# Optimization experiments

Hardware: AMD Instinct MI355X
Metric: run time of the kernel (lower is better)

The kernel has to match this reference:

```python
import jax, jax.numpy as jnp
import numpy as np

HEIGHT, WIDTH = 32, 32
NUM_HEADS = 16
FREQUENCY = 10000.0


def _get_thetas(dim, height, width, frequency):
    # dim = head_dim, must be even. Returns (height*width, dim).
    half = dim // 2
    ifreq = 1.0 / (frequency ** (jnp.arange(half, dtype=jnp.float32) / half))
    freqs_h = jnp.arange(height, dtype=jnp.float32)[:, None] * ifreq[None, :]  # (h, half)
    freqs_w = jnp.arange(width, dtype=jnp.float32)[:, None] * ifreq[None, :]   # (w, half)
    theta_h = jnp.broadcast_to(freqs_h[:, None, :], (height, width, half))
    theta_w = jnp.broadcast_to(freqs_w[None, :, :], (height, width, half))
    theta = jnp.concatenate([theta_h, theta_w], axis=-1)  # (h, w, dim)
    return theta.reshape(height * width, dim)


def _add_rope(t, cos, sin):
    # t: (b, h, n, d); cos/sin: (n, d) broadcast over batch and heads
    x1, x2 = jnp.split(t, 2, axis=-1)
    t_rot = jnp.concatenate([-x2, x1], axis=-1)
    return t * cos + t_rot * sin


def setup_inputs() -> dict:
    key = jax.random.key(0)
    k1, k2, k3 = jax.random.split(key, 3)
    b, n, c = 8, HEIGHT * WIDTH, 1024
    tensor = jax.random.normal(k1, (b, n, c), dtype=jnp.float32)
    w_qkv = jax.random.normal(k2, (3 * c, c), dtype=jnp.float32) * (c ** -0.5)
    w_proj = jax.random.normal(k3, (c, c), dtype=jnp.float32) * (c ** -0.5)
    return {"tensor": tensor, "w_qkv": w_qkv, "w_proj": w_proj}


def reference(tensor, w_qkv, w_proj):
    b, n, c = tensor.shape
    hd = c // NUM_HEADS
    # QKV projection, split per-head last dim into q,k,v (matches torch chunk on dim=-1)
    qkv = jnp.einsum('bnc,fc->bnf', tensor, w_qkv)            # (b, n, 3c)
    qkv = qkv.reshape(b, n, NUM_HEADS, 3 * hd).transpose(0, 2, 1, 3)  # (b, H, n, 3*hd)
    q, k, v = jnp.split(qkv, 3, axis=-1)                      # each (b, H, n, hd)
    # 2D RoPE on q, k
    theta = _get_thetas(hd, HEIGHT, WIDTH, FREQUENCY).astype(tensor.dtype)  # (n, hd)
    cos, sin = jnp.cos(theta), jnp.sin(theta)
    q = _add_rope(q, cos, sin)
    k = _add_rope(k, cos, sin)
    # scaled dot product attention
    scale = hd ** -0.5
    scores = jnp.einsum('bhqd,bhkd->bhqk', q, k) * scale
    attn = jax.nn.softmax(scores, axis=-1)
    o = jnp.einsum('bhqk,bhkd->bhqd', attn, v)
    o = o.transpose(0, 2, 1, 3).reshape(b, n, c)
    return jnp.einsum('bnc,oc->bno', o, w_proj)
```

## Files before the change

### kernel.cpp

```cpp
#include <hip/hip_runtime.h>

typedef __attribute__((ext_vector_type(8))) short short8v;
typedef __attribute__((ext_vector_type(4))) float floatx4;
typedef __attribute__((ext_vector_type(4))) unsigned short ushortx4;

__device__ __forceinline__ unsigned int f2bf(float f){
  unsigned int u = __float_as_uint(f);
  u += 0x7fffu + ((u >> 16) & 1u);
  return u >> 16;
}

__device__ __forceinline__ void gload_lds16(const void* g, void* l){
  __builtin_amdgcn_global_load_lds((const __attribute__((address_space(1))) void*)g,
                                   (__attribute__((address_space(3))) void*)l, 16, 0, 0);
}

__global__ __launch_bounds__(256) void prep(
    const floatx4* __restrict__ t,  ushortx4* __restrict__ dt,
    const floatx4* __restrict__ wq, ushortx4* __restrict__ dq,
    const floatx4* __restrict__ wp, ushortx4* __restrict__ dp,
    float2* __restrict__ cs)
{
  int i = blockIdx.x * 256 + threadIdx.x;
  if(i < 3145728){
    const floatx4* s; ushortx4* d; int j;
    if(i < 2097152){ s = t;  d = dt; j = i; }
    else if(i < 2883584){ s = wq; d = dq; j = i - 2097152; }
    else { s = wp; d = dp; j = i - 2883584; }
    floatx4 v = s[j];
    ushortx4 o;
    #pragma unroll
    for(int k = 0; k < 4; ++k) o[k] = (unsigned short)f2bf(v[k]);
    d[j] = o;
  } else {
    int j = i - 3145728;
    int p = j >> 6, dd = j & 63;
    int y = p >> 5, x = p & 31;
    int dm = dd & 31;
    float ifr = powf(10000.0f, -(float)dm * (1.0f / 32.0f));
    float th = (float)(dd < 32 ? y : x) * ifr;
    cs[j].x = cosf(th);
    cs[j].y = sinf(th);
  }
}

template<int EPI>
__global__ __launch_bounds__(512, 2) void gemm8(
    const unsigned short* __restrict__ A,
    const unsigned short* __restrict__ B,
    int K, int N, int NXB,
    float* __restrict__ Cf,
    const float2* __restrict__ cs,
    unsigned short* __restrict__ qw,
    unsigned short* __restrict__ kw,
    unsigned short* __restrict__ vtw)
{
  __shared__ char lds[147456];
  const int tid = threadIdx.x;
  const int w = tid >> 6, lane = tid & 63;
  const int g = lane >> 4, c0 = lane & 15;
  const int wm = w >> 2, wn = w & 3;
  const int NT = K >> 6;

  const int per = gridDim.x >> 3;
  const int wg = (blockIdx.x & 7) * per + (blockIdx.x >> 3);
  const int by = wg / NXB, bx = wg % NXB;
  const size_t m0 = (size_t)by * 128;
  const size_t n0 = (size_t)bx * 256;

  const int row0 = tid >> 2;
  const int xch = (tid & 3) ^ ((tid >> 3) & 3);
  const unsigned short* sA0 = A + (m0 + row0) * K + xch * 8;
  const unsigned short* sB0 = B + (n0 + row0) * K + xch * 8;
  const unsigned short* sB1 = B + (n0 + row0 + 128) * K + xch * 8;
  const int wb = w * 1024;

  auto stT = [&](int t, char* bp){
    gload_lds16(sA0 + t * 64,      bp + wb);
    gload_lds16(sA0 + t * 64 + 32, bp + 8192 + wb);
    gload_lds16(sB0 + t * 64,      bp + 16384 + wb);
    gload_lds16(sB1 + t * 64,      bp + 24576 + wb);
    gload_lds16(sB0 + t * 64 + 32, bp + 32768 + wb);
    gload_lds16(sB1 + t * 64 + 32, bp + 40960 + wb);
  };

  const int archy = (g ^ ((c0 >> 1) & 3)) << 4;
  auto rdA = [&](const char* bp, int kh, int mf) -> short8v {
    return *(const short8v*)(bp + kh * 8192 + (wm * 64 + mf * 16 + c0) * 64 + archy);
  };
  auto rdB = [&](const char* bp, int kh, int nf) -> short8v {
    return *(const short8v*)(bp + 16384 + kh * 16384 + (wn * 64 + nf * 16 + c0) * 64 + archy);
  };

  floatx4 acc[4][4] = {};

  stT(0, lds);
  stT(1, lds + 49152);
  asm volatile("s_waitcnt vmcnt(6)" ::: "memory");
  __builtin_amdgcn_s_barrier();
  __builtin_amdgcn_sched_barrier(0);

  char* pa_ = lds;
  char* pb_ = lds + 49152;
  char* pc_ = lds + 98304;
  for(int t = 0; t < NT; ++t){
    const int tn2 = (t + 2 < NT) ? t + 2 : NT - 1;
    short8v amA[4], bnA[4], amB[4], bnB[4];
    #pragma unroll
    for(int nf = 0; nf < 4; ++nf) bnA[nf] = rdB(pa_, 0, nf);
    #pragma unroll
    for(int mf = 0; mf < 4; ++mf) amA[mf] = rdA(pa_, 0, mf);
    #pragma unroll
    for(int nf = 0; nf < 4; ++nf) bnB[nf] = rdB(pa_, 1, nf);
    #pragma unroll
    for(int mf = 0; mf < 4; ++mf) amB[mf] = rdA(pa_, 1, mf);
    stT(tn2, pc_);
    __builtin_amdgcn_sched_barrier(0);
    __builtin_amdgcn_s_setprio(1);
    #pragma unroll
    for(int mf = 0; mf < 4; ++mf)
      #pragma unroll
      for(int nf = 0; nf < 4; ++nf)
        acc[mf][nf] = __builtin_amdgcn_mfma_f32_16x16x32_bf16(amA[mf], bnA[nf], acc[mf][nf], 0, 0, 0);
    #pragma unroll
    for(int mf = 0; mf < 4; ++mf)
      #pragma unroll
      for(int nf = 0; nf < 4; ++nf)
        acc[mf][nf] = __builtin_amdgcn_mfma_f32_16x16x32_bf16(amB[mf], bnB[nf], acc[mf][nf], 0, 0, 0);
    __builtin_amdgcn_s_setprio(0);
    asm volatile("s_waitcnt vmcnt(6)" ::: "memory");
    __builtin_amdgcn_s_barrier();
    __builtin_amdgcn_sched_barrier(0);
    char* tmp = pa_; pa_ = pb_; pb_ = pc_; pc_ = tmp;
  }
  __syncthreads();

  if(EPI == 0){
    #pragma unroll
    for(int mf = 0; mf < 4; ++mf){
      size_t mrow = m0 + wm * 64 + mf * 16 + g * 4;
      #pragma unroll
      for(int nf = 0; nf < 4; ++nf){
        size_t n = n0 + wn * 64 + nf * 16 + c0;
        #pragma unroll
        for(int r = 0; r < 4; ++r)
          Cf[(mrow + r) * N + n] = acc[mf][nf][r];
      }
    }
  } else {
    int t = (int)(n0 >> 6) + wn;
    int sect = t % 3, hh = t / 3;
    if(sect == 2){
      #pragma unroll
      for(int mf = 0; mf < 4; ++mf){
        size_t m = m0 + wm * 64 + mf * 16 + g * 4;
        int b = (int)(m >> 10); int p = (int)(m & 1023);
        #pragma unroll
        for(int nf = 0; nf < 4; ++nf){
          int d = nf * 16 + c0;
          ushortx4 pk;
          #pragma unroll
          for(int r = 0; r < 4; ++r) pk[r] = (unsigned short)f2bf(acc[mf][nf][r]);
          *(ushortx4*)(vtw + ((size_t)(b * 16 + hh) * 64 + d) * 1024 + p) = pk;
        }
      }
    } else {
      unsigned short* dst = (sect == 0) ? qw : kw;
      const float qs = (sect == 0) ? 0.18033688011112042f : 1.0f;
      const int codd = c0 & 1;
      #pragma unroll
      for(int mf = 0; mf < 4; ++mf){
        #pragma unroll
        for(int r = 0; r < 4; ++r){
          size_t m = m0 + wm * 64 + mf * 16 + g * 4 + r;
          int b = (int)(m >> 10); int p = (int)(m & 1023);
          const float2* csr = cs + (size_t)p * 64;
          unsigned short* orow = dst + ((size_t)(b * 16 + hh) * 1024 + p) * 64;
          #pragma unroll
          for(int nf = 0; nf < 2; ++nf){
            int d = nf * 16 + c0;
            float x1 = acc[mf][nf][r], x2 = acc[mf][nf + 2][r];
            float2 cc1 = csr[d], cc2 = csr[d + 32];
            unsigned int u1 = f2bf((x1 * cc1.x - x2 * cc1.y) * qs);
            unsigned int u2 = f2bf((x2 * cc2.x + x1 * cc2.y) * qs);
            unsigned int p1 = (unsigned int)__shfl_xor((int)u1, 1);
            unsigned int p2 = (unsigned int)__shfl_xor((int)u2, 1);
            unsigned int val = codd ? (p2 | (u2 << 16)) : (u1 | (p1 << 16));
            int off = codd ? (d + 31) : d;
            *(unsigned int*)(orow + off) = val;
          }
        }
      }
    }
  }
}

__global__ __launch_bounds__(512, 4) void attn_kernel(
    const unsigned short* __restrict__ qw,
    const unsigned short* __restrict__ kw,
    const unsigned short* __restrict__ vtw,
    unsigned short* __restrict__ ow)
{
  __shared__ char smem[65536];
  const int tid = threadIdx.x;
  const int w = tid >> 6, lane = tid & 63;
  const int g = lane >> 4, c0 = lane & 15;
  const int bb = blockIdx.x;
  const int xcd = bb & 7, slot = bb >> 3;
  const int bh = xcd + ((slot >> 2) << 3);
  const int qt = slot & 3;
  const size_t bhoff = (size_t)bh * 1024 * 64;
  const unsigned short* Qb = qw + bhoff;
  const unsigned short* Kb = kw + bhoff;
  const unsigned short* Vb = vtw + bhoff;
  const int q0 = qt * 256 + w * 32;
  char* Pw = smem + 32768 + w * 4096;

  const int srow = tid >> 3;
  const int sjx = ((tid & 7) ^ (srow & 7)) << 3;
  const unsigned short* ksrc = Kb + srow * 64 + sjx;
  const unsigned short* vsrc = Vb + (size_t)srow * 1024 + sjx;
  const int wbase = w * 1024;

  short8v bq[2][2];
  #pragma unroll
  for(int qf = 0; qf < 2; ++qf)
    #pragma unroll
    for(int i = 0; i < 2; ++i)
      bq[qf][i] = *(const short8v*)(Qb + (size_t)(q0 + qf * 16 + c0) * 64 + g * 8 + i * 32);

  floatx4 o[2][4] = {};
  float m_run[2] = {-1e30f, -1e30f};
  float l_part[2] = {0.0f, 0.0f};

  gload_lds16(ksrc, smem + wbase);
  gload_lds16(vsrc, smem + 8192 + wbase);
  __syncthreads();

  int cur = 0;
  for(int kv0 = 0; kv0 < 1024; kv0 += 64){
    char* Ksm = smem + cur * 16384;
    char* Vsm = smem + cur * 16384 + 8192;
    if(kv0 + 64 < 1024){
      char* alt = smem + (cur ^ 1) * 16384;
      gload_lds16(ksrc + (size_t)(kv0 + 64) * 64, alt + wbase);
      gload_lds16(vsrc + kv0 + 64, alt + 8192 + wbase);
    }
    floatx4 st[4][2];
    #pragma unroll
    for(int kf = 0; kf < 4; ++kf){
      const int krow = kf * 16 + c0;
      const char* kr = Ksm + (krow << 7);
      short8v ka0 = *(const short8v*)(kr + (((g    ) ^ (c0 & 7)) << 4));
      short8v ka1 = *(const short8v*)(kr + (((g + 4) ^ (c0 & 7)) << 4));
      #pragma unroll
      for(int qf = 0; qf < 2; ++qf){
        floatx4 z = {};
        z = __builtin_amdgcn_mfma_f32_16x16x32_bf16(ka0, bq[qf][0], z, 0, 0, 0);
        st[kf][qf] = __builtin_amdgcn_mfma_f32_16x16x32_bf16(ka1, bq[qf][1], z, 0, 0, 0);
      }
    }
    float vmax[2];
    #pragma unroll
    for(int qf = 0; qf < 2; ++qf){
      float vm = -1e30f;
      #pragma unroll
      for(int kf = 0; kf < 4; ++kf)
        #pragma unroll
        for(int r = 0; r < 4; ++r) vm = fmaxf(vm, st[kf][qf][r]);
      vm = fmaxf(vm, __shfl_xor(vm, 16));
      vm = fmaxf(vm, __shfl_xor(vm, 32));
      vmax[qf] = vm;
    }
    if(!__all(vmax[0] <= m_run[0] + 8.0f && vmax[1] <= m_run[1] + 8.0f)){
      #pragma unroll
      for(int qf = 0; qf < 2; ++qf){
        float m_new = fmaxf(m_run[qf], vmax[qf]);
        float sc = __builtin_amdgcn_exp2f(m_run[qf] - m_new);
        l_part[qf] *= sc;
        m_run[qf] = m_new;
        float f0 = __shfl(sc, g * 4 + 0);
        float f1 = __shfl(sc, g * 4 + 1);
        float f2 = __shfl(sc, g * 4 + 2);
        float f3 = __shfl(sc, g * 4 + 3);
        #pragma unroll
        for(int nf = 0; nf < 4; ++nf){
          o[qf][nf][0] *= f0; o[qf][nf][1] *= f1; o[qf][nf][2] *= f2; o[qf][nf][3] *= f3;
        }
      }
    }
    #pragma unroll
    for(int qf = 0; qf < 2; ++qf){
      float ps = 0.0f;
      #pragma unroll
      for(int kf = 0; kf < 4; ++kf){
        ushortx4 pk;
        #pragma unroll
        for(int r = 0; r < 4; ++r){
          float e = __builtin_amdgcn_exp2f(st[kf][qf][r] - m_run[qf]);
          ps += e;
          pk[r] = (unsigned short)f2bf(e);
        }
        int byo = (qf << 11) + (c0 << 7) + (kf << 5) + (g << 3);
        byo ^= (c0 & 7) << 4;
        *(ushortx4*)(Pw + byo) = pk;
      }
      l_part[qf] += ps;
    }
    short8v pa[2][2];
    #pragma unroll
    for(int mf = 0; mf < 2; ++mf)
      #pragma unroll
      for(int i = 0; i < 2; ++i){
        int byo = (mf << 11) + (c0 << 7) + (i << 6) + (g << 4);
        byo ^= (c0 & 7) << 4;
        pa[mf][i] = *(const short8v*)(Pw + byo);
      }
    #pragma unroll
    for(int nf = 0; nf < 4; ++nf){
      const int vrow = nf * 16 + c0;
      const char* vr = Vsm + (vrow << 7);
      short8v v0 = *(const short8v*)(vr + (((g    ) ^ (c0 & 7)) << 4));
      short8v v1 = *(const short8v*)(vr + (((g + 4) ^ (c0 & 7)) << 4));
      #pragma unroll
      for(int mf = 0; mf < 2; ++mf){
        o[mf][nf] = __builtin_amdgcn_mfma_f32_16x16x32_bf16(pa[mf][0], v0, o[mf][nf], 0, 0, 0);
        o[mf][nf] = __builtin_amdgcn_mfma_f32_16x16x32_bf16(pa[mf][1], v1, o[mf][nf], 0, 0, 0);
      }
    }
    __syncthreads();
    cur ^= 1;
  }

  const int b = bh >> 4, hh = bh & 15;
  #pragma unroll
  for(int mf = 0; mf < 2; ++mf){
    l_part[mf] += __shfl_xor(l_part[mf], 16);
    l_part[mf] += __shfl_xor(l_part[mf], 32);
    float i0 = 1.0f / __shfl(l_part[mf], g * 4 + 0);
    float i1 = 1.0f / __shfl(l_part[mf], g * 4 + 1);
    float i2 = 1.0f / __shfl(l_part[mf], g * 4 + 2);
    float i3 = 1.0f / __shfl(l_part[mf], g * 4 + 3);
    #pragma unroll
    for(int nf = 0; nf < 4; ++nf){
      o[mf][nf][0] *= i0; o[mf][nf][1] *= i1; o[mf][nf][2] *= i2; o[mf][nf][3] *= i3;
      #pragma unroll
      for(int r = 0; r < 4; ++r){
        size_t row = (size_t)b * 1024 + q0 + mf * 16 + g * 4 + r;
        ow[row * 1024 + hh * 64 + nf * 16 + c0] = (unsigned short)f2bf(o[mf][nf][r]);
      }
    }
  }
}


extern "C" void kernel_launch(void* const* d_in, const int* in_sizes, int n_in,
                              void* d_out, int out_size, void* d_ws, size_t ws_size,
                              hipStream_t stream){
  const float* tensor = (const float*)d_in[0];
  const float* w_qkv  = (const float*)d_in[1];
  const float* w_proj = (const float*)d_in[2];
  char* ws = (char*)d_ws;
  unsigned short* bfT  = (unsigned short*)(ws);
  unsigned short* bfWq = (unsigned short*)(ws + 16777216);
  unsigned short* bfWp = (unsigned short*)(ws + 23068672);
  float2*         cs   = (float2*)        (ws + 25165824);
  unsigned short* qw   = (unsigned short*)(ws + 25690112);
  unsigned short* kw   = (unsigned short*)(ws + 42467328);
  unsigned short* vtw  = (unsigned short*)(ws + 59244544);
  unsigned short* owp  = (unsigned short*)(ws + 76021760);

  prep<<<12544, 256, 0, stream>>>((const floatx4*)tensor, (ushortx4*)bfT,
                                  (const floatx4*)w_qkv,  (ushortx4*)bfWq,
                                  (const floatx4*)w_proj, (ushortx4*)bfWp, cs);

  gemm8<1><<<768, 512, 0, stream>>>(bfT, bfWq, 1024, 3072, 12,
                                    nullptr, cs, qw, kw, vtw);
  attn_kernel<<<512, 512, 0, stream>>>(qw, kw, vtw, owp);
  gemm8<0><<<256, 512, 0, stream>>>(owp, bfWp, 1024, 1024, 4,
                                    (float*)d_out, nullptr, nullptr, nullptr, nullptr);
}
```

Baseline: 160.9 us.

## Double-buffer GEMM fragment registers so LDS reads overlap MFMA work

Restructures the bf16 GEMM main loop to keep two sets of A/B fragment registers. While the MFMAs for the current tile run, the next tile's fragments are read from LDS, and the loop is unrolled by two to alternate between the register sets. The fine-grained `s_waitcnt vmcnt(6)` plus barrier is replaced by a plain `__syncthreads`. That forces each global-to-LDS prefetch to finish within one iteration, which shortens the effective prefetch depth, and the extra fragment set raises VGPR pressure. The loop also assumes NT is even.

```diff
diff --git a/kernel.cpp b/kernel.cpp
--- a/kernel.cpp
+++ b/kernel.cpp
@@ -85,55 +85,68 @@
   };
 
   const int archy = (g ^ ((c0 >> 1) & 3)) << 4;
-  auto rdA = [&](const char* bp, int kh, int mf) -> short8v {
-    return *(const short8v*)(bp + kh * 8192 + (wm * 64 + mf * 16 + c0) * 64 + archy);
+  auto rdSet = [&](const char* bp, short8v (&aA)[4], short8v (&bA)[4],
+                                   short8v (&aB)[4], short8v (&bB)[4]){
+    #pragma unroll
+    for(int nf = 0; nf < 4; ++nf)
+      bA[nf] = *(const short8v*)(bp + 16384 + (wn * 64 + nf * 16 + c0) * 64 + archy);
+    #pragma unroll
+    for(int mf = 0; mf < 4; ++mf)
+      aA[mf] = *(const short8v*)(bp + (wm * 64 + mf * 16 + c0) * 64 + archy);
+    #pragma unroll
+    for(int nf = 0; nf < 4; ++nf)
+      bB[nf] = *(const short8v*)(bp + 32768 + (wn * 64 + nf * 16 + c0) * 64 + archy);
+    #pragma unroll
+    for(int mf = 0; mf < 4; ++mf)
+      aB[mf] = *(const short8v*)(bp + 8192 + (wm * 64 + mf * 16 + c0) * 64 + archy);
   };
-  auto rdB = [&](const char* bp, int kh, int nf) -> short8v {
-    return *(const short8v*)(bp + 16384 + kh * 16384 + (wn * 64 + nf * 16 + c0) * 64 + archy);
+
+  floatx4 acc[4][4] = {};
+  auto mmaSet = [&](short8v (&aA)[4], short8v (&bA)[4],
+                    short8v (&aB)[4], short8v (&bB)[4]){
+    __builtin_amdgcn_s_setprio(1);
+    #pragma unroll
+    for(int mf = 0; mf < 4; ++mf)
+      #pragma unroll
+      for(int nf = 0; nf < 4; ++nf)
+        acc[mf][nf] = __builtin_amdgcn_mfma_f32_16x16x32_bf16(aA[mf], bA[nf], acc[mf][nf], 0, 0, 0);
+    #pragma unroll
+    for(int mf = 0; mf < 4; ++mf)
+      #pragma unroll
+      for(int nf = 0; nf < 4; ++nf)
+        acc[mf][nf] = __builtin_amdgcn_mfma_f32_16x16x32_bf16(aB[mf], bB[nf], acc[mf][nf], 0, 0, 0);
+    __builtin_amdgcn_s_setprio(0);
   };
 
-  floatx4 acc[4][4] = {};
+  short8v aA0[4], bA0[4], aB0[4], bB0[4];
+  short8v aA1[4], bA1[4], aB1[4], bB1[4];
 
   stT(0, lds);
   stT(1, lds + 49152);
-  asm volatile("s_waitcnt vmcnt(6)" ::: "memory");
-  __builtin_amdgcn_s_barrier();
-  __builtin_amdgcn_sched_barrier(0);
-
+  __syncthreads();
   char* pa_ = lds;
   char* pb_ = lds + 49152;
   char* pc_ = lds + 98304;
-  for(int t = 0; t < NT; ++t){
-    const int tn2 = (t + 2 < NT) ? t + 2 : NT - 1;
-    short8v amA[4], bnA[4], amB[4], bnB[4];
-    #pragma unroll
-    for(int nf = 0; nf < 4; ++nf) bnA[nf] = rdB(pa_, 0, nf);
-    #pragma unroll
-    for(int mf = 0; mf < 4; ++mf) amA[mf] = rdA(pa_, 0, mf);
-    #pragma unroll
-    for(int nf = 0; nf < 4; ++nf) bnB[nf] = rdB(pa_, 1, nf);
-    #pragma unroll
-    for(int mf = 0; mf < 4; ++mf) amB[mf] = rdA(pa_, 1, mf);
-    stT(tn2, pc_);
-    __builtin_amdgcn_sched_barrier(0);
-    __builtin_amdgcn_s_setprio(1);
-    #pragma unroll
-    for(int mf = 0; mf < 4; ++mf)
-      #pragma unroll
-      for(int nf = 0; nf < 4; ++nf)
-        acc[mf][nf] = __builtin_amdgcn_mfma_f32_16x16x32_bf16(amA[mf], bnA[nf], acc[mf][nf], 0, 0, 0);
-    #pragma unroll
-    for(int mf = 0; mf < 4; ++mf)
-      #pragma unroll
-      for(int nf = 0; nf < 4; ++nf)
-        acc[mf][nf] = __builtin_amdgcn_mfma_f32_16x16x32_bf16(amB[mf], bnB[nf], acc[mf][nf], 0, 0, 0);
-    __builtin_amdgcn_s_setprio(0);
-    asm volatile("s_waitcnt vmcnt(6)" ::: "memory");
-    __builtin_amdgcn_s_barrier();
-    __builtin_amdgcn_sched_barrier(0);
-    char* tmp = pa_; pa_ = pb_; pb_ = pc_; pc_ = tmp;
-  }
-  __syncthreads();
+  rdSet(pa_, aA0, bA0, aB0, bB0);
+
+  for(int t = 0; t < NT; t += 2){
+    {
+      const int tn = (t + 2 < NT) ? t + 2 : NT - 1;
+      stT(tn, pc_);
+      rdSet(pb_, aA1, bA1, aB1, bB1);
+      mmaSet(aA0, bA0, aB0, bB0);
+      __syncthreads();
+      char* tmp = pa_; pa_ = pb_; pb_ = pc_; pc_ = tmp;
+    }
+    {
+      const int tn = (t + 3 < NT) ? t + 3 : NT - 1;
+      stT(tn, pc_);
+      rdSet(pb_, aA0, bA0, aB0, bB0);
+      mmaSet(aA1, bA1, aB1, bB1);
+      __syncthreads();
+      char* tmp = pa_; pa_ = pb_; pb_ = pc_; pc_ = tmp;
+    }
+  }
 
   if(EPI == 0){
     #pragma unroll
```

Measured after the change: 162.5 us. About the same (+1.0%).
